# Kernel optimization log

Measured on AMD Instinct MI355X. Metric: run time of the kernel, lower is better.

## Reference

```python
import jax, jax.numpy as jnp
import numpy as np

B = 1024          # batch
INPUT_LEN = 4096  # dense width of incoming activation
OUT = 4096        # out_features
FAN_IN = 128      # in_features (fixed fan-in per output)


def setup_inputs() -> dict:
    key = jax.random.key(0)
    k1, k2, k3, k4 = jax.random.split(key, 4)
    bound = 1.0 / np.sqrt(FAN_IN)
    inp = jax.random.normal(k1, (B, INPUT_LEN), dtype=jnp.float32)
    weight = jax.random.uniform(k2, (OUT, FAN_IN), dtype=jnp.float32, minval=-bound, maxval=bound)
    bias = jax.random.uniform(k3, (OUT,), dtype=jnp.float32, minval=-bound, maxval=bound)
    indx_seqs = jax.random.randint(k4, (OUT, FAN_IN), 0, INPUT_LEN, dtype=jnp.int64 if jax.config.jax_enable_x64 else jnp.int32)
    return {"input": inp, "weight": weight, "bias": bias, "indx_seqs": indx_seqs}


def reference(input, weight, bias, indx_seqs):
    # gathered: (B, OUT, FAN_IN); weight broadcast over batch; reduce fan-in.
    gathered = input[:, indx_seqs]
    out = jnp.einsum('of,bof->bo', weight, gathered) + bias
    return out
```

## Files before the change

### kernel.cpp

```cpp
#include <hip/hip_runtime.h>
#include <stdint.h>

#define NB    1024
#define IL    4096
#define NOUT  4096
#define FI    128
#define BTILE 8
#define OSPLIT 4
#define OTILE (NOUT / OSPLIT)
#define SLAB_DW (IL * (BTILE / 2))
#define SLAB_BLOCKS ((NB / BTILE) * IL / 256)
#define PACK_BLOCKS (NOUT * FI / (256 * 4))

__device__ __forceinline__ uint32_t rne_bf16_hi(float x) {
  uint32_t u = __float_as_uint(x);
  u += 0x7FFFu + ((u >> 16) & 1u);
  return u & 0xFFFF0000u;
}

__global__ __launch_bounds__(256)
void prep_kernel(const float* __restrict__ in, uint32_t* __restrict__ slab,
                 const int* __restrict__ idx, const float* __restrict__ w,
                 uint32_t* __restrict__ pack) {
  const int bid = blockIdx.x;
  if (bid < SLAB_BLOCKS) {
    int t = bid * 256 + threadIdx.x;
    int g = t >> 12;
    int i = t & (IL - 1);
    const float* base = in + (size_t)g * (8 * IL) + i;
    uint4 v;
    v.x = rne_bf16_hi(base[1 * IL]) | (rne_bf16_hi(base[0 * IL]) >> 16);
    v.y = rne_bf16_hi(base[3 * IL]) | (rne_bf16_hi(base[2 * IL]) >> 16);
    v.z = rne_bf16_hi(base[5 * IL]) | (rne_bf16_hi(base[4 * IL]) >> 16);
    v.w = rne_bf16_hi(base[7 * IL]) | (rne_bf16_hi(base[6 * IL]) >> 16);
    reinterpret_cast<uint4*>(slab)[t] = v;
  } else {
    int t = (bid - SLAB_BLOCKS) * 256 + threadIdx.x;
    int4   iv = reinterpret_cast<const int4*>(idx)[t];
    float4 wv = reinterpret_cast<const float4*>(w)[t];
    uint4 p;
    p.x = rne_bf16_hi(wv.x) | (((uint32_t)iv.x << 4) & 0xFFFFu);
    p.y = rne_bf16_hi(wv.y) | (((uint32_t)iv.y << 4) & 0xFFFFu);
    p.z = rne_bf16_hi(wv.z) | (((uint32_t)iv.z << 4) & 0xFFFFu);
    p.w = rne_bf16_hi(wv.w) | (((uint32_t)iv.w << 4) & 0xFFFFu);
    reinterpret_cast<uint4*>(pack)[t] = p;
  }
}

template<int MODE>
__global__ __launch_bounds__(1024)
void lincond_kernel(const float* __restrict__ input,
                    const uint32_t* __restrict__ slab,
                    const uint32_t* __restrict__ pack,
                    const int*  __restrict__ idxs,
                    const float* __restrict__ wgt,
                    const float* __restrict__ bias,
                    float* __restrict__ out) {
  __shared__ uint32_t lds[SLAB_DW];
  const int bid   = blockIdx.x;
  const int b0    = (bid >> 2) * BTILE;
  const int obase = (bid & 3) * OTILE;
  const int tid   = threadIdx.x;

  if (MODE == 2) {
    const uint32_t* src = slab + (size_t)(b0 >> 3) * SLAB_DW;
    #pragma unroll
    for (int r = 0; r < 4; ++r) {
      int e = (r * 1024 + tid) * 4;
      __builtin_amdgcn_global_load_lds(
          (const __attribute__((address_space(1))) uint32_t*)(src + e),
          (__attribute__((address_space(3))) uint32_t*)(lds + e),
          16, 0, 0);
    }
  } else {
    #pragma unroll
    for (int rep = 0; rep < 16; ++rep) {
      int e = rep * 1024 + tid;
      int d = e >> 12;
      int i = e & (IL - 1);
      float x0 = input[(size_t)(b0 + 2 * d)     * IL + i];
      float x1 = input[(size_t)(b0 + 2 * d + 1) * IL + i];
      lds[i * 4 + d] = rne_bf16_hi(x1) | (rne_bf16_hi(x0) >> 16);
    }
  }
  __syncthreads();

  const int o = obase + tid;
  const char* ldsb = reinterpret_cast<const char*>(lds);
  float acc[8] = {0.f,0.f,0.f,0.f,0.f,0.f,0.f,0.f};

#define GBODY(OFF, WV) {                                          \
    uint4 g = *reinterpret_cast<const uint4*>(ldsb + (OFF));      \
    float wv = (WV);                                              \
    acc[0] = fmaf(wv, __uint_as_float(g.x << 16),         acc[0]);\
    acc[1] = fmaf(wv, __uint_as_float(g.x & 0xFFFF0000u), acc[1]);\
    acc[2] = fmaf(wv, __uint_as_float(g.y << 16),         acc[2]);\
    acc[3] = fmaf(wv, __uint_as_float(g.y & 0xFFFF0000u), acc[3]);\
    acc[4] = fmaf(wv, __uint_as_float(g.z << 16),         acc[4]);\
    acc[5] = fmaf(wv, __uint_as_float(g.z & 0xFFFF0000u), acc[5]);\
    acc[6] = fmaf(wv, __uint_as_float(g.w << 16),         acc[6]);\
    acc[7] = fmaf(wv, __uint_as_float(g.w & 0xFFFF0000u), acc[7]);}

#define PBODY(P) \
    GBODY((P.x & 0xFFFFu), __uint_as_float(P.x & 0xFFFF0000u)) \
    GBODY((P.y & 0xFFFFu), __uint_as_float(P.y & 0xFFFF0000u)) \
    GBODY((P.z & 0xFFFFu), __uint_as_float(P.z & 0xFFFF0000u)) \
    GBODY((P.w & 0xFFFFu), __uint_as_float(P.w & 0xFFFF0000u))

#define RBODY(IV, WV) \
    GBODY(((uint32_t)IV.x << 4), WV.x) \
    GBODY(((uint32_t)IV.y << 4), WV.y) \
    GBODY(((uint32_t)IV.z << 4), WV.z) \
    GBODY(((uint32_t)IV.w << 4), WV.w)

  if (MODE >= 1) {
    const uint4* pw = reinterpret_cast<const uint4*>(pack) + (size_t)o * (FI / 4);
    #pragma unroll 2
    for (int j = 0; j < 8; ++j) {
      uint4 p0 = pw[j * 4 + 0];
      uint4 p1 = pw[j * 4 + 1];
      uint4 p2 = pw[j * 4 + 2];
      uint4 p3 = pw[j * 4 + 3];
      PBODY(p0) PBODY(p1) PBODY(p2) PBODY(p3)
    }
  } else {
    const int4*   ip = reinterpret_cast<const int4*>(idxs)  + (size_t)o * (FI / 4);
    const float4* wp = reinterpret_cast<const float4*>(wgt) + (size_t)o * (FI / 4);
    #pragma unroll 2
    for (int j = 0; j < 8; ++j) {
      int4   i0 = ip[j * 4 + 0], i1 = ip[j * 4 + 1], i2 = ip[j * 4 + 2], i3 = ip[j * 4 + 3];
      float4 w0 = wp[j * 4 + 0], w1 = wp[j * 4 + 1], w2 = wp[j * 4 + 2], w3 = wp[j * 4 + 3];
      RBODY(i0, w0) RBODY(i1, w1) RBODY(i2, w2) RBODY(i3, w3)
    }
  }

  const float bv = bias[o];
  #pragma unroll
  for (int k = 0; k < 8; ++k) {
    out[(size_t)(b0 + k) * NOUT + o] = acc[k] + bv;
  }
}

extern "C" void kernel_launch(void* const* d_in, const int* in_sizes, int n_in,
                              void* d_out, int out_size, void* d_ws, size_t ws_size,
                              hipStream_t stream) {
  const float* input  = (const float*)d_in[0];
  const float* weight = (const float*)d_in[1];
  const float* bias   = (const float*)d_in[2];
  const int*   idxs   = (const int*)d_in[3];
  float*       out    = (float*)d_out;

  const size_t pack_bytes = (size_t)NOUT * FI * sizeof(uint32_t);
  const size_t slab_bytes = (size_t)(NB / BTILE) * SLAB_DW * sizeof(uint32_t);
  const int grid = (NB / BTILE) * OSPLIT;

  if (ws_size >= pack_bytes + slab_bytes) {
    uint32_t* pack = (uint32_t*)d_ws;
    uint32_t* slab = (uint32_t*)((char*)d_ws + pack_bytes);
    prep_kernel<<<SLAB_BLOCKS + PACK_BLOCKS, 256, 0, stream>>>(input, slab, idxs, weight, pack);
    lincond_kernel<2><<<grid, 1024, 0, stream>>>(input, slab, pack, nullptr, nullptr, bias, out);
  } else {
    lincond_kernel<0><<<grid, 1024, 0, stream>>>(input, nullptr, nullptr, idxs, weight, bias, out);
  }
}
```

Baseline: 54.31 us.

## Reorder packed index/weight entries per output to spread LDS bank accesses

The pack step now handles one output row per thread instead of a flat elementwise conversion. It permutes each row's 128 (index, weight) entries by the low 3 bits of the index, rotated by o&7. The aim is that at each inner-loop step, neighbouring threads read 16-byte LDS chunks in different bank groups, cutting LDS bank conflicts in the gather. In exchange the prep kernel does serial per-row work with strided, uncoalesced global reads and scattered writes, and only 16 blocks are launched for it, which may lengthen the prep stage.

Measured after the change: 116.1 us. +113.8%, slower.

```diff
diff --git a/kernel.cpp b/kernel.cpp
--- a/kernel.cpp
+++ b/kernel.cpp
@@ -10,7 +10,7 @@
 #define OTILE (NOUT / OSPLIT)
 #define SLAB_DW (IL * (BTILE / 2))
 #define SLAB_BLOCKS ((NB / BTILE) * IL / 256)
-#define PACK_BLOCKS (NOUT * FI / (256 * 4))
+#define SORT_BLOCKS (NOUT / 256)
 
 __device__ __forceinline__ uint32_t rne_bf16_hi(float x) {
   uint32_t u = __float_as_uint(x);
@@ -35,15 +35,40 @@
     v.w = rne_bf16_hi(base[7 * IL]) | (rne_bf16_hi(base[6 * IL]) >> 16);
     reinterpret_cast<uint4*>(slab)[t] = v;
   } else {
-    int t = (bid - SLAB_BLOCKS) * 256 + threadIdx.x;
-    int4   iv = reinterpret_cast<const int4*>(idx)[t];
-    float4 wv = reinterpret_cast<const float4*>(w)[t];
-    uint4 p;
-    p.x = rne_bf16_hi(wv.x) | (((uint32_t)iv.x << 4) & 0xFFFFu);
-    p.y = rne_bf16_hi(wv.y) | (((uint32_t)iv.y << 4) & 0xFFFFu);
-    p.z = rne_bf16_hi(wv.z) | (((uint32_t)iv.z << 4) & 0xFFFFu);
-    p.w = rne_bf16_hi(wv.w) | (((uint32_t)iv.w << 4) & 0xFFFFu);
-    reinterpret_cast<uint4*>(pack)[t] = p;
+    const int o = (bid - SLAB_BLOCKS) * 256 + threadIdx.x;
+    const int r = o & 7;
+    const int*   irow = idx + (size_t)o * FI;
+    const float* wrow = w   + (size_t)o * FI;
+    uint32_t* prow = pack + (size_t)o * FI;
+
+    uint64_t cnt = 0;
+    #pragma unroll 4
+    for (int j = 0; j < FI; ++j) cnt += 1ull << (8 * (irow[j] & 7));
+    uint64_t used = 0;
+    #pragma unroll
+    for (int g = 0; g < 8; ++g) {
+      uint32_t n = (uint32_t)((cnt >> (8 * g)) & 0xFFu);
+      used |= (uint64_t)(n < 16u ? n : 16u) << (8 * g);
+    }
+    uint64_t cur = 0;
+    int lc = 0;
+    int lt = (int)((used >> (8 * ((0 + r) & 7))) & 0xFFu);
+    #pragma unroll 4
+    for (int j = 0; j < FI; ++j) {
+      uint32_t iv = (uint32_t)irow[j];
+      int g = (int)(iv & 7u);
+      int k = (int)((cur >> (8 * g)) & 0xFFu);
+      cur += 1ull << (8 * g);
+      int p;
+      if (k < 16) {
+        p = ((g - r) & 7) + 8 * k;
+      } else {
+        while (lt >= 16) { ++lc; lt = (int)((used >> (8 * ((lc + r) & 7))) & 0xFFu); }
+        p = lc + 8 * lt;
+        ++lt;
+      }
+      prow[p] = rne_bf16_hi(wrow[j]) | ((iv << 4) & 0xFFFFu);
+    }
   }
 }
 
@@ -157,7 +182,7 @@
   if (ws_size >= pack_bytes + slab_bytes) {
     uint32_t* pack = (uint32_t*)d_ws;
     uint32_t* slab = (uint32_t*)((char*)d_ws + pack_bytes);
-    prep_kernel<<<SLAB_BLOCKS + PACK_BLOCKS, 256, 0, stream>>>(input, slab, idxs, weight, pack);
+    prep_kernel<<<SLAB_BLOCKS + SORT_BLOCKS, 256, 0, stream>>>(input, slab, idxs, weight, pack);
     lincond_kernel<2><<<grid, 1024, 0, stream>>>(input, slab, pack, nullptr, nullptr, bias, out);
   } else {
     lincond_kernel<0><<<grid, 1024, 0, stream>>>(input, nullptr, nullptr, idxs, weight, bias, out);
```

## Reorder packed index/weight entries per row to spread LDS bank accesses

Applied to the files above, without the earlier changes.

The pack step now sorts each output row's 128 (index, weight) pairs by LDS bank group (index mod 8), using wavefront ballots to compute ranks. Each slot position lands on a distinct bank group, rotated by the output row, with overflow entries filling leftover slots. The aim is to cut LDS bank conflicts when the lanes of a wavefront gather 16-byte slab entries at the same loop step. In exchange the prep kernel does more work: ballots, popcounts and a scattered write per element.

Result: no change. 55.26 us (+1.7%).

```diff
diff --git a/kernel.cpp b/kernel.cpp
--- a/kernel.cpp
+++ b/kernel.cpp
@@ -10,7 +10,7 @@
 #define OTILE (NOUT / OSPLIT)
 #define SLAB_DW (IL * (BTILE / 2))
 #define SLAB_BLOCKS ((NB / BTILE) * IL / 256)
-#define PACK_BLOCKS (NOUT * FI / (256 * 4))
+#define SORT_BLOCKS (NOUT / 4)
 
 __device__ __forceinline__ uint32_t rne_bf16_hi(float x) {
   uint32_t u = __float_as_uint(x);
@@ -35,15 +35,51 @@
     v.w = rne_bf16_hi(base[7 * IL]) | (rne_bf16_hi(base[6 * IL]) >> 16);
     reinterpret_cast<uint4*>(slab)[t] = v;
   } else {
-    int t = (bid - SLAB_BLOCKS) * 256 + threadIdx.x;
-    int4   iv = reinterpret_cast<const int4*>(idx)[t];
-    float4 wv = reinterpret_cast<const float4*>(w)[t];
-    uint4 p;
-    p.x = rne_bf16_hi(wv.x) | (((uint32_t)iv.x << 4) & 0xFFFFu);
-    p.y = rne_bf16_hi(wv.y) | (((uint32_t)iv.y << 4) & 0xFFFFu);
-    p.z = rne_bf16_hi(wv.z) | (((uint32_t)iv.z << 4) & 0xFFFFu);
-    p.w = rne_bf16_hi(wv.w) | (((uint32_t)iv.w << 4) & 0xFFFFu);
-    reinterpret_cast<uint4*>(pack)[t] = p;
+    const int o = (bid - SLAB_BLOCKS) * 4 + (threadIdx.x >> 6);
+    const unsigned lane = threadIdx.x & 63u;
+    const uint32_t r = (uint32_t)(o & 7);
+    const int*   irow = idx + (size_t)o * FI;
+    const float* wrow = w   + (size_t)o * FI;
+    uint32_t* prow = pack + (size_t)o * FI;
+
+    uint32_t i0 = (uint32_t)irow[lane], i1 = (uint32_t)irow[64 + lane];
+    uint32_t w0 = rne_bf16_hi(wrow[lane]), w1 = rne_bf16_hi(wrow[64 + lane]);
+    uint32_t k0 = i0 & 7u, k1 = i1 & 7u;
+    const uint64_t lt = (1ull << lane) - 1ull;
+
+    uint32_t rank0 = 0, rank1 = 0;
+    uint64_t cntp = 0;
+    #pragma unroll
+    for (int g = 0; g < 8; ++g) {
+      uint64_t b0 = __ballot(k0 == (uint32_t)g);
+      uint64_t b1 = __ballot(k1 == (uint32_t)g);
+      uint32_t c0 = (uint32_t)__popcll(b0);
+      if (k0 == (uint32_t)g) rank0 = (uint32_t)__popcll(b0 & lt);
+      if (k1 == (uint32_t)g) rank1 = c0 + (uint32_t)__popcll(b1 & lt);
+      cntp |= (uint64_t)(c0 + (uint32_t)__popcll(b1)) << (8 * g);
+    }
+    uint64_t ov0 = __ballot(rank0 >= 16u);
+    uint64_t ov1 = __ballot(rank1 >= 16u);
+    uint32_t ofr0 = (uint32_t)__popcll(ov0 & lt);
+    uint32_t ofr1 = (uint32_t)__popcll(ov0) + (uint32_t)__popcll(ov1 & lt);
+
+    auto place = [&](uint32_t k, uint32_t rank, uint32_t ofr) -> uint32_t {
+      if (rank < 16u) return ((k - r) & 7u) + 8u * rank;
+      uint32_t cum = 0, p = 0;
+      bool done = false;
+      #pragma unroll
+      for (int lc = 0; lc < 8; ++lc) {
+        uint32_t gl = ((uint32_t)lc + r) & 7u;
+        uint32_t c  = (uint32_t)((cntp >> (8 * gl)) & 0xFFu);
+        uint32_t u  = c < 16u ? c : 16u;
+        uint32_t lcnt = 16u - u;
+        if (!done && ofr < cum + lcnt) { p = (uint32_t)lc + 8u * (u + ofr - cum); done = true; }
+        cum += lcnt;
+      }
+      return p;
+    };
+    prow[place(k0, rank0, ofr0)] = w0 | ((i0 << 4) & 0xFFFFu);
+    prow[place(k1, rank1, ofr1)] = w1 | ((i1 << 4) & 0xFFFFu);
   }
 }
 
@@ -157,7 +193,7 @@
   if (ws_size >= pack_bytes + slab_bytes) {
     uint32_t* pack = (uint32_t*)d_ws;
     uint32_t* slab = (uint32_t*)((char*)d_ws + pack_bytes);
-    prep_kernel<<<SLAB_BLOCKS + PACK_BLOCKS, 256, 0, stream>>>(input, slab, idxs, weight, pack);
+    prep_kernel<<<SLAB_BLOCKS + SORT_BLOCKS, 256, 0, stream>>>(input, slab, idxs, weight, pack);
     lincond_kernel<2><<<grid, 1024, 0, stream>>>(input, slab, pack, nullptr, nullptr, bias, out);
   } else {
     lincond_kernel<0><<<grid, 1024, 0, stream>>>(input, nullptr, nullptr, idxs, weight, bias, out);
```
